# Kernel tuning notes

Hardware: AMD Instinct MI355X
Metric: run time of the kernel (lower is better)

## Reference

```python
import jax, jax.numpy as jnp
import numpy as np

M, N, D, B = 8192, 64, 1, 25

# ---- quaternion / dual-quaternion algebra (w, x, y, z convention) ----

def qmul(a, b):
    aw, av = a[..., :1], a[..., 1:]
    bw, bv = b[..., :1], b[..., 1:]
    w = aw * bw - jnp.sum(av * bv, -1, keepdims=True)
    v = aw * bv + bw * av + jnp.cross(av, bv)
    return jnp.concatenate([w, v], -1)

def qconj(q):
    return q * jnp.array([1.0, -1.0, -1.0, -1.0], q.dtype)

def qrotate(q, v):
    w, qv = q[..., :1], q[..., 1:]
    uv = jnp.cross(qv, v)
    return v + 2.0 * (w * uv + jnp.cross(qv, uv))

def dq_inverse(dq):
    return (qconj(dq[0]), qconj(dq[1]))

def dq_mul(a, b):
    return (qmul(a[0], b[0]), qmul(a[0], b[1]) + qmul(a[1], b[0]))

def dq_apply(dq, pts):
    qr, qd = dq
    t = 2.0 * qmul(qd, qconj(qr))[..., 1:]  # translation part
    return qrotate(qr, pts) + t


def setup_inputs() -> dict:
    key = jax.random.key(0)
    ks = jax.random.split(key, 4)

    def make_dq(k, pre):
        k1, k2 = jax.random.split(k)
        qr = jax.random.normal(k1, pre + (4,), jnp.float32)
        qr = qr / jnp.linalg.norm(qr, axis=-1, keepdims=True)
        t = 0.2 * jax.random.normal(k2, pre + (3,), jnp.float32)
        tq = jnp.concatenate([jnp.zeros(pre + (1,), jnp.float32), t], -1)
        return qr, 0.5 * qmul(tq, qr)  # unit dual quaternion

    xyz = 0.3 * jax.random.normal(ks[0], (M, N, D, 3), jnp.float32)
    t_qr, t_qd = make_dq(ks[1], (M, B))
    r_qr, r_qd = make_dq(ks[2], (1, B))  # rest pose shared across frames, then expanded
    rest_qr = jnp.broadcast_to(r_qr, (M, B, 4))
    rest_qd = jnp.broadcast_to(r_qd, (M, B, 4))
    log_gauss = jnp.log(0.03) * jnp.ones((B, 3), jnp.float32) \
        + 0.1 * jax.random.normal(ks[3], (B, 3), jnp.float32)
    return {"xyz": xyz, "t_qr": t_qr, "t_qd": t_qd,
            "rest_qr": rest_qr, "rest_qd": rest_qd, "log_gauss": log_gauss}


def reference(xyz, t_qr, t_qd, rest_qr, rest_qd, log_gauss):
    # type == 'forward': se3 maps rest pose -> time-t pose
    t_art = (t_qr, t_qd)
    rest_art = (rest_qr, rest_qd)
    se3 = dq_mul(t_art, dq_inverse(rest_art))  # ((M,B,4),(M,B,4))

    # SkinningField: Gaussian bone influence in rest-bone coordinates
    art = (rest_qr[:, None, None], rest_qd[:, None, None])  # (M,1,1,B,4)
    xyz_bone = dq_apply(dq_inverse(art), xyz[..., None, :])  # (M,N,D,B,3)
    scale = jnp.exp(log_gauss)  # (B,3) per-bone anisotropic gauss scale
    dist2 = jnp.sum((xyz_bone / scale) ** 2, -1)  # (M,N,D,B)
    skin_prob = jax.nn.softmax(-0.5 * dist2, -1)  # softmax over bones

    # dual-quaternion blend skinning: sign-align to first bone, blend, normalize
    sign = jnp.sign(jnp.sum(se3[0] * se3[0][:, :1], -1, keepdims=True))
    sign = jnp.where(sign == 0, 1.0, sign)
    qr_s, qd_s = se3[0] * sign, se3[1] * sign
    qr_b = jnp.einsum('mndb,mbk->mndk', skin_prob, qr_s)  # (M,N,D,4)
    qd_b = jnp.einsum('mndb,mbk->mndk', skin_prob, qd_s)
    norm = jnp.linalg.norm(qr_b, axis=-1, keepdims=True)
    out = dq_apply((qr_b / norm, qd_b / norm), xyz)  # (M,N,D,3)
    return out
```

## Files before the change

### kernel.cpp

```cpp
#include <hip/hip_runtime.h>
#include <hip/hip_fp16.h>
#include <math.h>

#define MM 8192
#define NN 64
#define NB 25
#define MPB 16
#define PPT 4
#define LOG2E 1.44269504088896340736f

struct Q { float w, x, y, z; };

__device__ __forceinline__ Q qmul(const Q a, const Q b) {
    Q r;
    r.w = a.w*b.w - a.x*b.x - a.y*b.y - a.z*b.z;
    r.x = a.w*b.x + b.w*a.x + a.y*b.z - a.z*b.y;
    r.y = a.w*b.y + b.w*a.y + a.z*b.x - a.x*b.z;
    r.z = a.w*b.z + b.w*a.z + a.x*b.y - a.y*b.x;
    return r;
}

__device__ __forceinline__ unsigned pk_rn(float a, float b) {
    return __builtin_bit_cast(unsigned, __floats2half2_rn(a, b));
}

typedef __fp16 f16x2 __attribute__((ext_vector_type(2)));
__device__ __forceinline__ __half2 pk_rtz(float a, float b) {
    f16x2 v = __builtin_amdgcn_cvt_pkrtz(a, b);
    return __builtin_bit_cast(__half2, v);
}
__device__ __forceinline__ __half2 bc_h2(unsigned u) {
    return __builtin_bit_cast(__half2, u);
}

__global__ __launch_bounds__(256, 2) void skin_kernel(
    const float* __restrict__ xyz,
    const float* __restrict__ t_qr,
    const float* __restrict__ t_qd,
    const float* __restrict__ rest_qr,
    const float* __restrict__ rest_qd,
    const float* __restrict__ log_gauss,
    float* __restrict__ out)
{
    __shared__ __align__(16) float   kK[NB][12];
    __shared__ __align__(16) float   sref[MPB][4];
    __shared__ __align__(16) unsigned qQ[MPB][NB][4];

    const int t  = threadIdx.x;
    const int m0 = blockIdx.x * MPB;

    if (t < NB) {
        const int b = t;
        const float4 Rqv = *reinterpret_cast<const float4*>(rest_qr + b * 4);
        const float4 Rdv = *reinterpret_cast<const float4*>(rest_qd + b * 4);
        const Q Rq{Rqv.x, Rqv.y, Rqv.z, Rqv.w};
        const Q Rqc{Rq.w, -Rq.x, -Rq.y, -Rq.z};
        const Q Rdc{Rdv.x, -Rdv.y, -Rdv.z, -Rdv.w};
        const float i0 = __expf(-log_gauss[b * 3 + 0]);
        const float i1 = __expf(-log_gauss[b * 3 + 1]);
        const float i2 = __expf(-log_gauss[b * 3 + 2]);
        const Q tqb = qmul(Rdc, Rq);
        const float qw = Rqc.w, qx = Rqc.x, qy = Rqc.y, qz = Rqc.z;
        const float r00 = 1.f - 2.f*(qy*qy + qz*qz), r01 = 2.f*(qx*qy - qw*qz), r02 = 2.f*(qx*qz + qw*qy);
        const float r10 = 2.f*(qx*qy + qw*qz), r11 = 1.f - 2.f*(qx*qx + qz*qz), r12 = 2.f*(qy*qz - qw*qx);
        const float r20 = 2.f*(qx*qz - qw*qy), r21 = 2.f*(qy*qz + qw*qx), r22 = 1.f - 2.f*(qx*qx + qy*qy);
        const float g00 = r00*i0, g01 = r01*i0, g02 = r02*i0;
        const float g10 = r10*i1, g11 = r11*i1, g12 = r12*i1;
        const float g20 = r20*i2, g21 = r21*i2, g22 = r22*i2;
        const float u0 = 2.f*tqb.x*i0, u1 = 2.f*tqb.y*i1, u2 = 2.f*tqb.z*i2;
        const float c = LOG2E;
        kK[b][0] = -0.5f*c*(g00*g00 + g10*g10 + g20*g20);
        kK[b][1] = -0.5f*c*(g01*g01 + g11*g11 + g21*g21);
        kK[b][2] = -0.5f*c*(g02*g02 + g12*g12 + g22*g22);
        kK[b][3] = -c*(g00*g01 + g10*g11 + g20*g21);
        kK[b][4] = -c*(g00*g02 + g10*g12 + g20*g22);
        kK[b][5] = -c*(g01*g02 + g11*g12 + g21*g22);
        kK[b][6] = -c*(g00*u0 + g10*u1 + g20*u2);
        kK[b][7] = -c*(g01*u0 + g11*u1 + g21*u2);
        kK[b][8] = -c*(g02*u0 + g12*u1 + g22*u2);
        kK[b][9] = -0.5f*c*(u0*u0 + u1*u1 + u2*u2);
    }

    Q se_r1{0,0,0,0}, se_d1{0,0,0,0}, se_r2{0,0,0,0}, se_d2{0,0,0,0};
    int ms1 = 0, b1 = 0, ms2 = 0, b2 = 0;
    {
        const int r = t;
        ms1 = r / NB; b1 = r - ms1 * NB;
        const int gbase = (m0 * NB + r) * 4;
        const float4 Tqv = *reinterpret_cast<const float4*>(t_qr + gbase);
        const float4 Tdv = *reinterpret_cast<const float4*>(t_qd + gbase);
        const float4 Rqv = *reinterpret_cast<const float4*>(rest_qr + b1 * 4);
        const float4 Rdv = *reinterpret_cast<const float4*>(rest_qd + b1 * 4);
        const Q Tq{Tqv.x, Tqv.y, Tqv.z, Tqv.w};
        const Q Td{Tdv.x, Tdv.y, Tdv.z, Tdv.w};
        const Q Rq{Rqv.x, Rqv.y, Rqv.z, Rqv.w};
        const Q Rqc{Rq.w, -Rq.x, -Rq.y, -Rq.z};
        const Q Rdc{Rdv.x, -Rdv.y, -Rdv.z, -Rdv.w};
        se_r1 = qmul(Tq, Rqc);
        const Q a1 = qmul(Tq, Rdc);
        const Q a2 = qmul(Td, Rqc);
        se_d1 = Q{a1.w + a2.w, a1.x + a2.x, a1.y + a2.y, a1.z + a2.z};
        if (b1 == 0) *reinterpret_cast<float4*>(sref[ms1]) = make_float4(se_r1.w, se_r1.x, se_r1.y, se_r1.z);
    }
    const bool has2 = (t + 256) < (MPB * NB);
    if (has2) {
        const int r = t + 256;
        ms2 = r / NB; b2 = r - ms2 * NB;
        const int gbase = (m0 * NB + r) * 4;
        const float4 Tqv = *reinterpret_cast<const float4*>(t_qr + gbase);
        const float4 Tdv = *reinterpret_cast<const float4*>(t_qd + gbase);
        const float4 Rqv = *reinterpret_cast<const float4*>(rest_qr + b2 * 4);
        const float4 Rdv = *reinterpret_cast<const float4*>(rest_qd + b2 * 4);
        const Q Tq{Tqv.x, Tqv.y, Tqv.z, Tqv.w};
        const Q Td{Tdv.x, Tdv.y, Tdv.z, Tdv.w};
        const Q Rq{Rqv.x, Rqv.y, Rqv.z, Rqv.w};
        const Q Rqc{Rq.w, -Rq.x, -Rq.y, -Rq.z};
        const Q Rdc{Rdv.x, -Rdv.y, -Rdv.z, -Rdv.w};
        se_r2 = qmul(Tq, Rqc);
        const Q a1 = qmul(Tq, Rdc);
        const Q a2 = qmul(Td, Rqc);
        se_d2 = Q{a1.w + a2.w, a1.x + a2.x, a1.y + a2.y, a1.z + a2.z};
        if (b2 == 0) *reinterpret_cast<float4*>(sref[ms2]) = make_float4(se_r2.w, se_r2.x, se_r2.y, se_r2.z);
    }
    __syncthreads();

    {
        const float4 rf = *reinterpret_cast<const float4*>(sref[ms1]);
        const float d0 = se_r1.w*rf.x + se_r1.x*rf.y + se_r1.y*rf.z + se_r1.z*rf.w;
        const float sg = (d0 < 0.f) ? -1.f : 1.f;
        qQ[ms1][b1][0] = pk_rn(sg*se_r1.w, sg*se_r1.x);
        qQ[ms1][b1][1] = pk_rn(sg*se_r1.y, sg*se_r1.z);
        qQ[ms1][b1][2] = pk_rn(sg*se_d1.w, sg*se_d1.x);
        qQ[ms1][b1][3] = pk_rn(sg*se_d1.y, sg*se_d1.z);
    }
    if (has2) {
        const float4 rf = *reinterpret_cast<const float4*>(sref[ms2]);
        const float d0 = se_r2.w*rf.x + se_r2.x*rf.y + se_r2.y*rf.z + se_r2.z*rf.w;
        const float sg = (d0 < 0.f) ? -1.f : 1.f;
        qQ[ms2][b2][0] = pk_rn(sg*se_r2.w, sg*se_r2.x);
        qQ[ms2][b2][1] = pk_rn(sg*se_r2.y, sg*se_r2.z);
        qQ[ms2][b2][2] = pk_rn(sg*se_d2.w, sg*se_d2.x);
        qQ[ms2][b2][3] = pk_rn(sg*se_d2.y, sg*se_d2.z);
    }
    __syncthreads();

    const int m_sub = t >> 4;
    const int pt0   = (t & 15) * PPT;
    const int m     = m0 + m_sub;
    const int pbase = (m * NN + pt0) * 3;

    const float4 v0 = *reinterpret_cast<const float4*>(xyz + pbase);
    const float4 v1 = *reinterpret_cast<const float4*>(xyz + pbase + 4);
    const float4 v2 = *reinterpret_cast<const float4*>(xyz + pbase + 8);
    float px[PPT], py[PPT], pz[PPT];
    px[0]=v0.x; py[0]=v0.y; pz[0]=v0.z;
    px[1]=v0.w; py[1]=v1.x; pz[1]=v1.y;
    px[2]=v1.z; py[2]=v1.w; pz[2]=v2.x;
    px[3]=v2.y; py[3]=v2.z; pz[3]=v2.w;

    float fxx[PPT], fyy[PPT], fzz[PPT], fxy[PPT], fxz[PPT], fyz[PPT];
#pragma unroll
    for (int p = 0; p < PPT; ++p) {
        fxx[p]=px[p]*px[p]; fyy[p]=py[p]*py[p]; fzz[p]=pz[p]*pz[p];
        fxy[p]=px[p]*py[p]; fxz[p]=px[p]*pz[p]; fyz[p]=py[p]*pz[p];
    }

    float lg[PPT][NB];
    float mx[PPT] = {-3.4e38f, -3.4e38f, -3.4e38f, -3.4e38f};
#pragma unroll
    for (int b = 0; b < NB; ++b) {
        const float k0=kK[b][0], k1=kK[b][1], k2=kK[b][2], k3=kK[b][3], k4=kK[b][4];
        const float k5=kK[b][5], k6=kK[b][6], k7=kK[b][7], k8=kK[b][8], k9=kK[b][9];
#pragma unroll
        for (int p = 0; p < PPT; ++p) {
            float s = fmaf(k8, pz[p], k9);
            s = fmaf(k7, py[p], s);
            s = fmaf(k6, px[p], s);
            s = fmaf(k5, fyz[p], s);
            s = fmaf(k4, fxz[p], s);
            s = fmaf(k3, fxy[p], s);
            s = fmaf(k2, fzz[p], s);
            s = fmaf(k1, fyy[p], s);
            s = fmaf(k0, fxx[p], s);
            lg[p][b] = s;
            mx[p] = fmaxf(mx[p], s);
        }
    }

    const __half2 hz = __floats2half2_rn(0.f, 0.f);
    __half2 acc[PPT][4];
#pragma unroll
    for (int p = 0; p < PPT; ++p) { acc[p][0]=hz; acc[p][1]=hz; acc[p][2]=hz; acc[p][3]=hz; }

#pragma unroll
    for (int b = 0; b < NB; ++b) {
        const uint4 qv = *reinterpret_cast<const uint4*>(&qQ[m_sub][b][0]);
        const __half2 h0 = bc_h2(qv.x), h1 = bc_h2(qv.y), h2 = bc_h2(qv.z), h3 = bc_h2(qv.w);
#pragma unroll
        for (int p = 0; p < PPT; ++p) {
            const float e = __builtin_amdgcn_exp2f(lg[p][b] - mx[p]);
            const __half2 e2 = pk_rtz(e, e);
            acc[p][0] = __hfma2(e2, h0, acc[p][0]);
            acc[p][1] = __hfma2(e2, h1, acc[p][1]);
            acc[p][2] = __hfma2(e2, h2, acc[p][2]);
            acc[p][3] = __hfma2(e2, h3, acc[p][3]);
        }
    }

    float o[12];
#pragma unroll
    for (int p = 0; p < PPT; ++p) {
        const float aw = __low2float(acc[p][0]), ax = __high2float(acc[p][0]);
        const float ay = __low2float(acc[p][1]), az = __high2float(acc[p][1]);
        const float bw = __low2float(acc[p][2]), bx = __high2float(acc[p][2]);
        const float by = __low2float(acc[p][3]), bz = __high2float(acc[p][3]);

        const float inv = rsqrtf(aw*aw + ax*ax + ay*ay + az*az);
        const Q qr{aw*inv, ax*inv, ay*inv, az*inv};
        const Q qd{bw*inv, bx*inv, by*inv, bz*inv};
        const Q qrc{qr.w, -qr.x, -qr.y, -qr.z};
        const Q tq = qmul(qd, qrc);

        const float uvx = qr.y*pz[p] - qr.z*py[p];
        const float uvy = qr.z*px[p] - qr.x*pz[p];
        const float uvz = qr.x*py[p] - qr.y*px[p];
        const float cx = qr.y*uvz - qr.z*uvy;
        const float cy = qr.z*uvx - qr.x*uvz;
        const float cz = qr.x*uvy - qr.y*uvx;

        o[p*3+0] = px[p] + 2.f*(qr.w*uvx + cx) + 2.f*tq.x;
        o[p*3+1] = py[p] + 2.f*(qr.w*uvy + cy) + 2.f*tq.y;
        o[p*3+2] = pz[p] + 2.f*(qr.w*uvz + cz) + 2.f*tq.z;
    }

    *reinterpret_cast<float4*>(out + pbase)     = make_float4(o[0], o[1], o[2],  o[3]);
    *reinterpret_cast<float4*>(out + pbase + 4) = make_float4(o[4], o[5], o[6],  o[7]);
    *reinterpret_cast<float4*>(out + pbase + 8) = make_float4(o[8], o[9], o[10], o[11]);
}

extern "C" void kernel_launch(void* const* d_in, const int* in_sizes, int n_in,
                              void* d_out, int out_size, void* d_ws, size_t ws_size,
                              hipStream_t stream) {
    const float* xyz       = (const float*)d_in[0];
    const float* t_qr      = (const float*)d_in[1];
    const float* t_qd      = (const float*)d_in[2];
    const float* rest_qr   = (const float*)d_in[3];
    const float* rest_qd   = (const float*)d_in[4];
    const float* log_gauss = (const float*)d_in[5];
    float* out = (float*)d_out;

    hipLaunchKernelGGL(skin_kernel, dim3(MM / MPB), dim3(256), 0, stream,
                       xyz, t_qr, t_qd, rest_qr, rest_qd, log_gauss, out);
}
```

Before: 15.63 us.

## Split bone-constant prep into separate kernel and halve per-thread point work

Moves the per-bone Gaussian quadratic-form constants into a tiny prep kernel that writes to workspace; the main kernel then reads them from global memory instead of recomputing them into shared memory in every block. Blocks now cover 8 frames with 2 points per thread instead of 16 frames with 4, which doubles the grid and raises the occupancy hint to 4 waves. The xyz load is also issued before the se3 setup so its latency overlaps that work. The cost is a second launch plus scalar/global constant loads, and less per-thread reuse of the bone quaternions and constants.

```diff
diff --git a/kernel.cpp b/kernel.cpp
--- a/kernel.cpp
+++ b/kernel.cpp
@@ -5,8 +5,9 @@
 #define MM 8192
 #define NN 64
 #define NB 25
-#define MPB 16
-#define PPT 4
+#define MPB 8
+#define PPT 2
+#define KS 12
 #define LOG2E 1.44269504088896340736f
 
 struct Q { float w, x, y, z; };
@@ -33,130 +34,104 @@
     return __builtin_bit_cast(__half2, u);
 }
 
-__global__ __launch_bounds__(256, 2) void skin_kernel(
+__global__ __launch_bounds__(64) void prep_kernel(
+    const float* __restrict__ rest_qr, const float* __restrict__ rest_qd,
+    const float* __restrict__ log_gauss, float* __restrict__ Kbuf)
+{
+    const int b = threadIdx.x;
+    if (b >= NB) return;
+    const float4 Rqv = *reinterpret_cast<const float4*>(rest_qr + b * 4);
+    const float4 Rdv = *reinterpret_cast<const float4*>(rest_qd + b * 4);
+    const Q Rq{Rqv.x, Rqv.y, Rqv.z, Rqv.w};
+    const Q Rqc{Rq.w, -Rq.x, -Rq.y, -Rq.z};
+    const Q Rdc{Rdv.x, -Rdv.y, -Rdv.z, -Rdv.w};
+    const float i0 = __expf(-log_gauss[b * 3 + 0]);
+    const float i1 = __expf(-log_gauss[b * 3 + 1]);
+    const float i2 = __expf(-log_gauss[b * 3 + 2]);
+    const Q tqb = qmul(Rdc, Rq);
+    const float qw = Rqc.w, qx = Rqc.x, qy = Rqc.y, qz = Rqc.z;
+    const float r00 = 1.f - 2.f*(qy*qy + qz*qz), r01 = 2.f*(qx*qy - qw*qz), r02 = 2.f*(qx*qz + qw*qy);
+    const float r10 = 2.f*(qx*qy + qw*qz), r11 = 1.f - 2.f*(qx*qx + qz*qz), r12 = 2.f*(qy*qz - qw*qx);
+    const float r20 = 2.f*(qx*qz - qw*qy), r21 = 2.f*(qy*qz + qw*qx), r22 = 1.f - 2.f*(qx*qx + qy*qy);
+    const float g00 = r00*i0, g01 = r01*i0, g02 = r02*i0;
+    const float g10 = r10*i1, g11 = r11*i1, g12 = r12*i1;
+    const float g20 = r20*i2, g21 = r21*i2, g22 = r22*i2;
+    const float u0 = 2.f*tqb.x*i0, u1 = 2.f*tqb.y*i1, u2 = 2.f*tqb.z*i2;
+    const float c = LOG2E;
+    float* kp = Kbuf + b * KS;
+    *reinterpret_cast<float4*>(kp + 0) = make_float4(
+        -0.5f*c*(g00*g00 + g10*g10 + g20*g20),
+        -0.5f*c*(g01*g01 + g11*g11 + g21*g21),
+        -0.5f*c*(g02*g02 + g12*g12 + g22*g22),
+        -c*(g00*g01 + g10*g11 + g20*g21));
+    *reinterpret_cast<float4*>(kp + 4) = make_float4(
+        -c*(g00*g02 + g10*g12 + g20*g22),
+        -c*(g01*g02 + g11*g12 + g21*g22),
+        -c*(g00*u0 + g10*u1 + g20*u2),
+        -c*(g01*u0 + g11*u1 + g21*u2));
+    *reinterpret_cast<float4*>(kp + 8) = make_float4(
+        -c*(g02*u0 + g12*u1 + g22*u2),
+        -0.5f*c*(u0*u0 + u1*u1 + u2*u2), 0.f, 0.f);
+}
+
+__global__ __launch_bounds__(256, 4) void skin_kernel(
     const float* __restrict__ xyz,
     const float* __restrict__ t_qr,
     const float* __restrict__ t_qd,
     const float* __restrict__ rest_qr,
     const float* __restrict__ rest_qd,
-    const float* __restrict__ log_gauss,
+    const float* __restrict__ Kb,
     float* __restrict__ out)
 {
-    __shared__ __align__(16) float   kK[NB][12];
-    __shared__ __align__(16) float   sref[MPB][4];
+    __shared__ __align__(16) float    sref[MPB][4];
     __shared__ __align__(16) unsigned qQ[MPB][NB][4];
 
     const int t  = threadIdx.x;
     const int m0 = blockIdx.x * MPB;
 
-    if (t < NB) {
-        const int b = t;
-        const float4 Rqv = *reinterpret_cast<const float4*>(rest_qr + b * 4);
-        const float4 Rdv = *reinterpret_cast<const float4*>(rest_qd + b * 4);
-        const Q Rq{Rqv.x, Rqv.y, Rqv.z, Rqv.w};
-        const Q Rqc{Rq.w, -Rq.x, -Rq.y, -Rq.z};
-        const Q Rdc{Rdv.x, -Rdv.y, -Rdv.z, -Rdv.w};
-        const float i0 = __expf(-log_gauss[b * 3 + 0]);
-        const float i1 = __expf(-log_gauss[b * 3 + 1]);
-        const float i2 = __expf(-log_gauss[b * 3 + 2]);
-        const Q tqb = qmul(Rdc, Rq);
-        const float qw = Rqc.w, qx = Rqc.x, qy = Rqc.y, qz = Rqc.z;
-        const float r00 = 1.f - 2.f*(qy*qy + qz*qz), r01 = 2.f*(qx*qy - qw*qz), r02 = 2.f*(qx*qz + qw*qy);
-        const float r10 = 2.f*(qx*qy + qw*qz), r11 = 1.f - 2.f*(qx*qx + qz*qz), r12 = 2.f*(qy*qz - qw*qx);
-        const float r20 = 2.f*(qx*qz - qw*qy), r21 = 2.f*(qy*qz + qw*qx), r22 = 1.f - 2.f*(qx*qx + qy*qy);
-        const float g00 = r00*i0, g01 = r01*i0, g02 = r02*i0;
-        const float g10 = r10*i1, g11 = r11*i1, g12 = r12*i1;
-        const float g20 = r20*i2, g21 = r21*i2, g22 = r22*i2;
-        const float u0 = 2.f*tqb.x*i0, u1 = 2.f*tqb.y*i1, u2 = 2.f*tqb.z*i2;
-        const float c = LOG2E;
-        kK[b][0] = -0.5f*c*(g00*g00 + g10*g10 + g20*g20);
-        kK[b][1] = -0.5f*c*(g01*g01 + g11*g11 + g21*g21);
-        kK[b][2] = -0.5f*c*(g02*g02 + g12*g12 + g22*g22);
-        kK[b][3] = -c*(g00*g01 + g10*g11 + g20*g21);
-        kK[b][4] = -c*(g00*g02 + g10*g12 + g20*g22);
-        kK[b][5] = -c*(g01*g02 + g11*g12 + g21*g22);
-        kK[b][6] = -c*(g00*u0 + g10*u1 + g20*u2);
-        kK[b][7] = -c*(g01*u0 + g11*u1 + g21*u2);
-        kK[b][8] = -c*(g02*u0 + g12*u1 + g22*u2);
-        kK[b][9] = -0.5f*c*(u0*u0 + u1*u1 + u2*u2);
-    }
-
-    Q se_r1{0,0,0,0}, se_d1{0,0,0,0}, se_r2{0,0,0,0}, se_d2{0,0,0,0};
-    int ms1 = 0, b1 = 0, ms2 = 0, b2 = 0;
-    {
-        const int r = t;
-        ms1 = r / NB; b1 = r - ms1 * NB;
-        const int gbase = (m0 * NB + r) * 4;
+    const int m_sub = t >> 5;
+    const int pt0   = (t & 31) * PPT;
+    const int pbase = ((m0 + m_sub) * NN + pt0) * 3;
+    const float2 a0 = *reinterpret_cast<const float2*>(xyz + pbase);
+    const float2 a1 = *reinterpret_cast<const float2*>(xyz + pbase + 2);
+    const float2 a2 = *reinterpret_cast<const float2*>(xyz + pbase + 4);
+
+    Q se_r{0,0,0,0}, se_d{0,0,0,0};
+    int ms = 0, bb = 0;
+    const bool act = t < MPB * NB;
+    if (act) {
+        ms = t / NB; bb = t - ms * NB;
+        const int gbase = (m0 * NB + t) * 4;
         const float4 Tqv = *reinterpret_cast<const float4*>(t_qr + gbase);
         const float4 Tdv = *reinterpret_cast<const float4*>(t_qd + gbase);
-        const float4 Rqv = *reinterpret_cast<const float4*>(rest_qr + b1 * 4);
-        const float4 Rdv = *reinterpret_cast<const float4*>(rest_qd + b1 * 4);
+        const float4 Rqv = *reinterpret_cast<const float4*>(rest_qr + bb * 4);
+        const float4 Rdv = *reinterpret_cast<const float4*>(rest_qd + bb * 4);
         const Q Tq{Tqv.x, Tqv.y, Tqv.z, Tqv.w};
         const Q Td{Tdv.x, Tdv.y, Tdv.z, Tdv.w};
         const Q Rq{Rqv.x, Rqv.y, Rqv.z, Rqv.w};
         const Q Rqc{Rq.w, -Rq.x, -Rq.y, -Rq.z};
         const Q Rdc{Rdv.x, -Rdv.y, -Rdv.z, -Rdv.w};
-        se_r1 = qmul(Tq, Rqc);
-        const Q a1 = qmul(Tq, Rdc);
-        const Q a2 = qmul(Td, Rqc);
-        se_d1 = Q{a1.w + a2.w, a1.x + a2.x, a1.y + a2.y, a1.z + a2.z};
-        if (b1 == 0) *reinterpret_cast<float4*>(sref[ms1]) = make_float4(se_r1.w, se_r1.x, se_r1.y, se_r1.z);
-    }
-    const bool has2 = (t + 256) < (MPB * NB);
-    if (has2) {
-        const int r = t + 256;
-        ms2 = r / NB; b2 = r - ms2 * NB;
-        const int gbase = (m0 * NB + r) * 4;
-        const float4 Tqv = *reinterpret_cast<const float4*>(t_qr + gbase);
-        const float4 Tdv = *reinterpret_cast<const float4*>(t_qd + gbase);
-        const float4 Rqv = *reinterpret_cast<const float4*>(rest_qr + b2 * 4);
-        const float4 Rdv = *reinterpret_cast<const float4*>(rest_qd + b2 * 4);
-        const Q Tq{Tqv.x, Tqv.y, Tqv.z, Tqv.w};
-        const Q Td{Tdv.x, Tdv.y, Tdv.z, Tdv.w};
-        const Q Rq{Rqv.x, Rqv.y, Rqv.z, Rqv.w};
-        const Q Rqc{Rq.w, -Rq.x, -Rq.y, -Rq.z};
-        const Q Rdc{Rdv.x, -Rdv.y, -Rdv.z, -Rdv.w};
-        se_r2 = qmul(Tq, Rqc);
-        const Q a1 = qmul(Tq, Rdc);
-        const Q a2 = qmul(Td, Rqc);
-        se_d2 = Q{a1.w + a2.w, a1.x + a2.x, a1.y + a2.y, a1.z + a2.z};
-        if (b2 == 0) *reinterpret_cast<float4*>(sref[ms2]) = make_float4(se_r2.w, se_r2.x, se_r2.y, se_r2.z);
+        se_r = qmul(Tq, Rqc);
+        const Q a1q = qmul(Tq, Rdc);
+        const Q a2q = qmul(Td, Rqc);
+        se_d = Q{a1q.w + a2q.w, a1q.x + a2q.x, a1q.y + a2q.y, a1q.z + a2q.z};
+        if (bb == 0) *reinterpret_cast<float4*>(sref[ms]) = make_float4(se_r.w, se_r.x, se_r.y, se_r.z);
     }
     __syncthreads();
-
-    {
-        const float4 rf = *reinterpret_cast<const float4*>(sref[ms1]);
-        const float d0 = se_r1.w*rf.x + se_r1.x*rf.y + se_r1.y*rf.z + se_r1.z*rf.w;
+    if (act) {
+        const float4 rf = *reinterpret_cast<const float4*>(sref[ms]);
+        const float d0 = se_r.w*rf.x + se_r.x*rf.y + se_r.y*rf.z + se_r.z*rf.w;
         const float sg = (d0 < 0.f) ? -1.f : 1.f;
-        qQ[ms1][b1][0] = pk_rn(sg*se_r1.w, sg*se_r1.x);
-        qQ[ms1][b1][1] = pk_rn(sg*se_r1.y, sg*se_r1.z);
-        qQ[ms1][b1][2] = pk_rn(sg*se_d1.w, sg*se_d1.x);
-        qQ[ms1][b1][3] = pk_rn(sg*se_d1.y, sg*se_d1.z);
-    }
-    if (has2) {
-        const float4 rf = *reinterpret_cast<const float4*>(sref[ms2]);
-        const float d0 = se_r2.w*rf.x + se_r2.x*rf.y + se_r2.y*rf.z + se_r2.z*rf.w;
-        const float sg = (d0 < 0.f) ? -1.f : 1.f;
-        qQ[ms2][b2][0] = pk_rn(sg*se_r2.w, sg*se_r2.x);
-        qQ[ms2][b2][1] = pk_rn(sg*se_r2.y, sg*se_r2.z);
-        qQ[ms2][b2][2] = pk_rn(sg*se_d2.w, sg*se_d2.x);
-        qQ[ms2][b2][3] = pk_rn(sg*se_d2.y, sg*se_d2.z);
+        qQ[ms][bb][0] = pk_rn(sg*se_r.w, sg*se_r.x);
+        qQ[ms][bb][1] = pk_rn(sg*se_r.y, sg*se_r.z);
+        qQ[ms][bb][2] = pk_rn(sg*se_d.w, sg*se_d.x);
+        qQ[ms][bb][3] = pk_rn(sg*se_d.y, sg*se_d.z);
     }
     __syncthreads();
 
-    const int m_sub = t >> 4;
-    const int pt0   = (t & 15) * PPT;
-    const int m     = m0 + m_sub;
-    const int pbase = (m * NN + pt0) * 3;
-
-    const float4 v0 = *reinterpret_cast<const float4*>(xyz + pbase);
-    const float4 v1 = *reinterpret_cast<const float4*>(xyz + pbase + 4);
-    const float4 v2 = *reinterpret_cast<const float4*>(xyz + pbase + 8);
     float px[PPT], py[PPT], pz[PPT];
-    px[0]=v0.x; py[0]=v0.y; pz[0]=v0.z;
-    px[1]=v0.w; py[1]=v1.x; pz[1]=v1.y;
-    px[2]=v1.z; py[2]=v1.w; pz[2]=v2.x;
-    px[3]=v2.y; py[3]=v2.z; pz[3]=v2.w;
+    px[0]=a0.x; py[0]=a0.y; pz[0]=a1.x;
+    px[1]=a1.y; py[1]=a2.x; pz[1]=a2.y;
 
     float fxx[PPT], fyy[PPT], fzz[PPT], fxy[PPT], fxz[PPT], fyz[PPT];
 #pragma unroll
@@ -166,11 +141,11 @@
     }
 
     float lg[PPT][NB];
-    float mx[PPT] = {-3.4e38f, -3.4e38f, -3.4e38f, -3.4e38f};
+    float mx[PPT] = {-3.4e38f, -3.4e38f};
 #pragma unroll
     for (int b = 0; b < NB; ++b) {
-        const float k0=kK[b][0], k1=kK[b][1], k2=kK[b][2], k3=kK[b][3], k4=kK[b][4];
-        const float k5=kK[b][5], k6=kK[b][6], k7=kK[b][7], k8=kK[b][8], k9=kK[b][9];
+        const float k0=Kb[b*KS+0], k1=Kb[b*KS+1], k2=Kb[b*KS+2], k3=Kb[b*KS+3], k4=Kb[b*KS+4];
+        const float k5=Kb[b*KS+5], k6=Kb[b*KS+6], k7=Kb[b*KS+7], k8=Kb[b*KS+8], k9=Kb[b*KS+9];
 #pragma unroll
         for (int p = 0; p < PPT; ++p) {
             float s = fmaf(k8, pz[p], k9);
@@ -207,7 +182,7 @@
         }
     }
 
-    float o[12];
+    float o[PPT*3];
 #pragma unroll
     for (int p = 0; p < PPT; ++p) {
         const float aw = __low2float(acc[p][0]), ax = __high2float(acc[p][0]);
@@ -233,9 +208,9 @@
         o[p*3+2] = pz[p] + 2.f*(qr.w*uvz + cz) + 2.f*tq.z;
     }
 
-    *reinterpret_cast<float4*>(out + pbase)     = make_float4(o[0], o[1], o[2],  o[3]);
-    *reinterpret_cast<float4*>(out + pbase + 4) = make_float4(o[4], o[5], o[6],  o[7]);
-    *reinterpret_cast<float4*>(out + pbase + 8) = make_float4(o[8], o[9], o[10], o[11]);
+    *reinterpret_cast<float2*>(out + pbase)     = make_float2(o[0], o[1]);
+    *reinterpret_cast<float2*>(out + pbase + 2) = make_float2(o[2], o[3]);
+    *reinterpret_cast<float2*>(out + pbase + 4) = make_float2(o[4], o[5]);
 }
 
 extern "C" void kernel_launch(void* const* d_in, const int* in_sizes, int n_in,
@@ -247,8 +222,11 @@
     const float* rest_qr   = (const float*)d_in[3];
     const float* rest_qd   = (const float*)d_in[4];
     const float* log_gauss = (const float*)d_in[5];
-    float* out = (float*)d_out;
-
+    float* out  = (float*)d_out;
+    float* Kbuf = (float*)d_ws;
+
+    hipLaunchKernelGGL(prep_kernel, dim3(1), dim3(64), 0, stream,
+                       rest_qr, rest_qd, log_gauss, Kbuf);
     hipLaunchKernelGGL(skin_kernel, dim3(MM / MPB), dim3(256), 0, stream,
-                       xyz, t_qr, t_qd, rest_qr, rest_qd, log_gauss, out);
-}
+                       xyz, t_qr, t_qd, rest_qr, rest_qd, Kbuf, out);
+}
```

Measured after the change: 20.82 us. 33.2% more time.

## Fuse logit and blend passes with an online-softmax running max

Applied to the files above, without the earlier changes.

Merges the two bone loops into one that computes each bone's Gaussian logit and immediately folds it into the half-precision accumulators, rescaling them whenever a new running maximum appears. This removes the per-thread 4x25 logit array, lowering register pressure and possibly raising occupancy. In exchange it adds an extra exp2, a packed multiply and max bookkeeping per bone per point, and repeated fp16 rescaling may change rounding slightly.

```diff
diff --git a/kernel.cpp b/kernel.cpp
--- a/kernel.cpp
+++ b/kernel.cpp
@@ -146,8 +146,7 @@
 
     const int m_sub = t >> 4;
     const int pt0   = (t & 15) * PPT;
-    const int m     = m0 + m_sub;
-    const int pbase = (m * NN + pt0) * 3;
+    const int pbase = ((m0 + m_sub) * NN + pt0) * 3;
 
     const float4 v0 = *reinterpret_cast<const float4*>(xyz + pbase);
     const float4 v1 = *reinterpret_cast<const float4*>(xyz + pbase + 4);
@@ -165,12 +164,13 @@
         fxy[p]=px[p]*py[p]; fxz[p]=px[p]*pz[p]; fyz[p]=py[p]*pz[p];
     }
 
-    float lg[PPT][NB];
-    float mx[PPT] = {-3.4e38f, -3.4e38f, -3.4e38f, -3.4e38f};
-#pragma unroll
-    for (int b = 0; b < NB; ++b) {
-        const float k0=kK[b][0], k1=kK[b][1], k2=kK[b][2], k3=kK[b][3], k4=kK[b][4];
-        const float k5=kK[b][5], k6=kK[b][6], k7=kK[b][7], k8=kK[b][8], k9=kK[b][9];
+    float M[PPT];
+    __half2 acc[PPT][4];
+
+    {
+        const uint4 qv = *reinterpret_cast<const uint4*>(&qQ[m_sub][0][0]);
+        const float k0=kK[0][0], k1=kK[0][1], k2=kK[0][2], k3=kK[0][3], k4=kK[0][4];
+        const float k5=kK[0][5], k6=kK[0][6], k7=kK[0][7], k8=kK[0][8], k9=kK[0][9];
 #pragma unroll
         for (int p = 0; p < PPT; ++p) {
             float s = fmaf(k8, pz[p], k9);
@@ -182,28 +182,42 @@
             s = fmaf(k2, fzz[p], s);
             s = fmaf(k1, fyy[p], s);
             s = fmaf(k0, fxx[p], s);
-            lg[p][b] = s;
-            mx[p] = fmaxf(mx[p], s);
+            M[p] = s;
+            acc[p][0] = bc_h2(qv.x);
+            acc[p][1] = bc_h2(qv.y);
+            acc[p][2] = bc_h2(qv.z);
+            acc[p][3] = bc_h2(qv.w);
         }
     }
 
-    const __half2 hz = __floats2half2_rn(0.f, 0.f);
-    __half2 acc[PPT][4];
-#pragma unroll
-    for (int p = 0; p < PPT; ++p) { acc[p][0]=hz; acc[p][1]=hz; acc[p][2]=hz; acc[p][3]=hz; }
-
-#pragma unroll
-    for (int b = 0; b < NB; ++b) {
+#pragma unroll
+    for (int b = 1; b < NB; ++b) {
         const uint4 qv = *reinterpret_cast<const uint4*>(&qQ[m_sub][b][0]);
         const __half2 h0 = bc_h2(qv.x), h1 = bc_h2(qv.y), h2 = bc_h2(qv.z), h3 = bc_h2(qv.w);
+        const float k0=kK[b][0], k1=kK[b][1], k2=kK[b][2], k3=kK[b][3], k4=kK[b][4];
+        const float k5=kK[b][5], k6=kK[b][6], k7=kK[b][7], k8=kK[b][8], k9=kK[b][9];
 #pragma unroll
         for (int p = 0; p < PPT; ++p) {
-            const float e = __builtin_amdgcn_exp2f(lg[p][b] - mx[p]);
+            float s = fmaf(k8, pz[p], k9);
+            s = fmaf(k7, py[p], s);
+            s = fmaf(k6, px[p], s);
+            s = fmaf(k5, fyz[p], s);
+            s = fmaf(k4, fxz[p], s);
+            s = fmaf(k3, fxy[p], s);
+            s = fmaf(k2, fzz[p], s);
+            s = fmaf(k1, fyy[p], s);
+            s = fmaf(k0, fxx[p], s);
+            const float d  = s - M[p];
+            const float dp = fmaxf(d, 0.f);
+            M[p] += dp;
+            const float e  = __builtin_amdgcn_exp2f(d - dp);
+            const float sc = __builtin_amdgcn_exp2f(-dp);
             const __half2 e2 = pk_rtz(e, e);
-            acc[p][0] = __hfma2(e2, h0, acc[p][0]);
-            acc[p][1] = __hfma2(e2, h1, acc[p][1]);
-            acc[p][2] = __hfma2(e2, h2, acc[p][2]);
-            acc[p][3] = __hfma2(e2, h3, acc[p][3]);
+            const __half2 s2 = pk_rtz(sc, sc);
+            acc[p][0] = __hfma2(acc[p][0], s2, __hmul2(e2, h0));
+            acc[p][1] = __hfma2(acc[p][1], s2, __hmul2(e2, h1));
+            acc[p][2] = __hfma2(acc[p][2], s2, __hmul2(e2, h2));
+            acc[p][3] = __hfma2(acc[p][3], s2, __hmul2(e2, h3));
         }
     }
 
```

After: 19.08 us. 1.22x slower.
